# Performance work log

Measured on AMD Instinct MI355X. Metric: run time of the kernel, lower is better.

The kernel has to match this reference:

```python
import jax, jax.numpy as jnp
import numpy as np

B, N, D, F_IN, E, RATIO, C, HEADS, KERNELS = 128, 512, 128, 128, 524288, 128, 10, 4, 3
ALPHA = 0.5


def setup_inputs() -> dict:
    key = jax.random.key(0)
    ks = jax.random.split(key, 20)

    def w(k, shape, fan):
        return (jax.random.normal(k, shape, jnp.float32) / np.float32(np.sqrt(fan)))

    gid = jnp.arange(E, dtype=jnp.int32) // (E // B)
    src = gid * N + jax.random.randint(ks[0], (E,), 0, N, dtype=jnp.int32)
    dst = gid * N + jax.random.randint(ks[1], (E,), 0, N, dtype=jnp.int32)
    edge_index = jnp.stack([src, dst]).astype(jnp.int32)
    return {
        'x': jax.random.normal(ks[2], (B * N, F_IN), jnp.float32),
        'edge_index': edge_index,
        'enc_w': w(ks[3], (F_IN, D), F_IN), 'enc_b': jnp.zeros((D,), jnp.float32),
        'gconv_w': w(ks[4], (3, KERNELS, D, D), D), 'gconv_b': jnp.zeros((3, KERNELS, D), jnp.float32),
        'wg1_w': w(ks[5], (D,), D), 'wg1_b': jnp.zeros((1,), jnp.float32),
        'wg2_w': w(ks[6], (D,), D), 'wg2_b': jnp.zeros((1,), jnp.float32),
        'pg1_w': w(ks[7], (D,), D), 'pg1_b': jnp.zeros((1,), jnp.float32),
        'pg2_w': w(ks[8], (D,), D), 'pg2_b': jnp.zeros((1,), jnp.float32),
        'q_w': w(ks[9], (D, D), D), 'q_b': jnp.zeros((D,), jnp.float32),
        'k_w': w(ks[10], (D, D), D), 'k_b': jnp.zeros((D,), jnp.float32),
        'v_w': w(ks[11], (D, D), D), 'v_b': jnp.zeros((D,), jnp.float32),
        'o_w': w(ks[12], (D, D), D), 'o_b': jnp.zeros((D,), jnp.float32),
        'ro_w': w(ks[13], (RATIO,), RATIO), 'ro_b': jnp.zeros((1,), jnp.float32),
        'c1_w': w(ks[14], (D, D), D), 'c1_b': jnp.zeros((D,), jnp.float32),
        'c2_w': w(ks[15], (D, C), D), 'c2_b': jnp.zeros((C,), jnp.float32),
    }


def _make_gcn(edge_index, n):
    # PyG GCNConv: add self-loops, symmetric normalization D^-1/2 (A+I) D^-1/2
    src, dst = edge_index[0], edge_index[1]
    deg = jax.ops.segment_sum(jnp.ones(src.shape[0], jnp.float32), dst, num_segments=n) + 1.0
    dinv = jax.lax.rsqrt(deg)
    norm = dinv[src] * dinv[dst]          # [E]
    self_norm = dinv * dinv               # self-loop coefficient

    def gcn(x, W, b):
        h = x @ W                                                  # [n, out]
        out = jax.ops.segment_sum(h[src] * norm[:, None], dst, num_segments=n)
        return out + h * self_norm[:, None] + b
    return gcn


def _forward(x, edge_index, enc_w, enc_b, gconv_w, gconv_b,
             wg1_w, wg1_b, wg2_w, wg2_b, pg1_w, pg1_b, pg2_w, pg2_b,
             q_w, q_b, k_w, k_b, v_w, v_b, o_w, o_b, ro_w, ro_b,
             c1_w, c1_b, c2_w, c2_b):
    n = x.shape[0]
    gcn = _make_gcn(edge_index, n)
    h = x @ enc_w + enc_b                   # node encoder (dropout: eval mode)

    def mkgc(hin, Ws, bs):                  # sum of relu(GCNConv) over kernels
        out = jax.nn.relu(gcn(hin, Ws[0], bs[0]))
        for kk in range(1, Ws.shape[0]):
            out = out + jax.nn.relu(gcn(hin, Ws[kk], bs[kk]))
        return out

    x1 = mkgc(h, gconv_w[0], gconv_b[0])
    x2 = mkgc(x1, gconv_w[1], gconv_b[1])
    x3 = mkgc(x2, gconv_w[2], gconv_b[2])

    def gla_score(xi, w1, b1, w2, b2):      # GLAPool(flag=1): global + local score
        s1 = xi @ w1[:, None] + b1          # [n,1]
        s2 = gcn(xi, w2[:, None], b2)       # [n,1]
        return ALPHA * s1 + (1.0 - ALPHA) * s2

    wts = jnp.concatenate([gla_score(xi, wg1_w, wg1_b, wg2_w, wg2_b)
                           for xi in (x1, x2, x3)], axis=-1)        # [n,3]
    wts = jax.nn.softmax(wts, axis=-1)
    xf = wts[:, 0:1] * x1 + wts[:, 1:2] * x2 + wts[:, 2:3] * x3

    # GLAPool top-k pooling (uniform graph sizes -> dense [B,N])
    score = gla_score(xf, pg1_w, pg1_b, pg2_w, pg2_b)[:, 0].reshape(B, N)
    vals, idx = jax.lax.top_k(score, RATIO)                          # [B,RATIO]
    xd = xf.reshape(B, N, D)
    xp = jnp.take_along_axis(xd, idx[:, :, None], axis=1) * jnp.tanh(vals)[:, :, None]

    # MAB: Q from pooled nodes, K/V = GCNConv over full graph
    dh = D // HEADS
    Qh = (xp @ q_w + q_b).reshape(B, RATIO, HEADS, dh)
    K = gcn(xf, k_w, k_b).reshape(B, N, HEADS, dh)
    V = gcn(xf, v_w, v_b).reshape(B, N, HEADS, dh)
    att = jnp.einsum('bqhd,bkhd->bhqk', Qh, K) / jnp.sqrt(jnp.float32(D))
    A = jax.nn.softmax(att, axis=-1)
    O = Qh + jnp.einsum('bhqk,bkhd->bqhd', A, V)
    O = O.reshape(B, RATIO, D)
    O = O + jax.nn.relu(O @ o_w + o_b)

    # Conv1d(ratio, 1, 1) readout == learned weighted sum over pooled slots
    xg = jnp.einsum('r,brd->bd', ro_w, O) + ro_b                     # [B,D]

    hc = jax.nn.relu(xg @ c1_w + c1_b)
    logp = jax.nn.log_softmax(hc @ c2_w + c2_b, axis=-1)
    return logp, xg


def reference(x, edge_index, enc_w, enc_b, gconv_w, gconv_b,
              wg1_w, wg1_b, wg2_w, wg2_b, pg1_w, pg1_b, pg2_w, pg2_b,
              q_w, q_b, k_w, k_b, v_w, v_b, o_w, o_b, ro_w, ro_b,
              c1_w, c1_b, c2_w, c2_b):
    return _forward(x, edge_index, enc_w, enc_b, gconv_w, gconv_b,
                    wg1_w, wg1_b, wg2_w, wg2_b, pg1_w, pg1_b, pg2_w, pg2_b,
                    q_w, q_b, k_w, k_b, v_w, v_b, o_w, o_b, ro_w, ro_b,
                    c1_w, c1_b, c2_w, c2_b)
```

## Files before the change

kernel.cpp:

```cpp
#include <hip/hip_runtime.h>
#include <math.h>

#define N_NODES 65536
#define NE      524288
#define DD      128
#define BGRAPH  128
#define NPG     512
#define RATIO_K 128
#define NHEAD   4
#define DHEAD   32

typedef short bf16x8 __attribute__((ext_vector_type(8)));
typedef float f32x4 __attribute__((ext_vector_type(4)));

union U8 { unsigned short u[8]; bf16x8 v; };
union U4x { unsigned q[4]; bf16x8 v; };

__device__ __forceinline__ unsigned short f2b(float f) {
  unsigned u = __float_as_uint(f);
  unsigned r = u + 0x7fffu + ((u >> 16) & 1u);
  return (unsigned short)(r >> 16);
}
__device__ __forceinline__ float b2f(unsigned short h) {
  return __uint_as_float(((unsigned)h) << 16);
}
__device__ __forceinline__ void split3t(float v, unsigned short& h, unsigned short& m, unsigned short& l) {
  unsigned u = __float_as_uint(v);
  h = (unsigned short)(u >> 16);
  float vm = v - __uint_as_float(u & 0xffff0000u);
  unsigned um = __float_as_uint(vm);
  m = (unsigned short)(um >> 16);
  float vl = vm - __uint_as_float(um & 0xffff0000u);
  l = (unsigned short)(__float_as_uint(vl) >> 16);
}


__global__ void count_kernel(const int* __restrict__ dst, int* __restrict__ cnt) {
  int e = blockIdx.x * 256 + threadIdx.x;
  if (e < NE) atomicAdd(&cnt[dst[e]], 1);
}

__global__ void dinv_kernel(const int* __restrict__ cnt, float* __restrict__ dinv) {
  int i = blockIdx.x * 256 + threadIdx.x;
  if (i < N_NODES) dinv[i] = rsqrtf((float)cnt[i] + 1.0f);
}

__global__ __launch_bounds__(512) void scan_kernel2(const int* __restrict__ cnt, int* __restrict__ rp) {
  __shared__ int part[512];
  int g = blockIdx.x, t = threadIdx.x;
  int v = cnt[g * 512 + t];
  part[t] = v;
  __syncthreads();
  for (int off = 1; off < 512; off <<= 1) {
    int u = (t >= off) ? part[t - off] : 0;
    __syncthreads();
    part[t] += u;
    __syncthreads();
  }
  rp[g * 512 + t] = g * 4096 + part[t] - v;
  if (g == BGRAPH - 1 && t == 511) rp[N_NODES] = NE;
}

__global__ void scatter_kernel(const int* __restrict__ edge, const int* __restrict__ rp,
                               int* __restrict__ fill, const float* __restrict__ dinv,
                               int* __restrict__ col, float* __restrict__ wgt) {
  int e = blockIdx.x * 256 + threadIdx.x;
  if (e >= NE) return;
  int s = edge[e];
  int d = edge[NE + e];
  int p = rp[d] + atomicAdd(&fill[d], 1);
  col[p] = s;
  wgt[p] = dinv[s] * dinv[d];
}

struct WPtrs { const float* p[14]; };

__global__ void wprep_all(WPtrs wp, unsigned short* __restrict__ dstBase) {
  int mat = blockIdx.y;
  int idx = blockIdx.x * 256 + threadIdx.x;
  const float* __restrict__ W = wp.p[mat];
  unsigned short* __restrict__ dst = dstBase + (size_t)mat * 49152;
  int k = idx >> 7, n = idx & 127;
  float v = W[k * 128 + n];
  unsigned short h, m, l;
  split3t(v, h, m, l);
  dst[n * 128 + k] = h;
  dst[16384 + n * 128 + k] = m;
  dst[32768 + n * 128 + k] = l;
}

#define WROW 36

template<int NW, bool RELU, bool RES, bool DUAL, bool DOT>
__global__ __launch_bounds__(256, 2) void mfma_gemm8(
    const float* __restrict__ A,
    const unsigned short* __restrict__ Wt,
    const float* __restrict__ bias, const float* __restrict__ bias2,
    const float* __restrict__ res,
    float* __restrict__ out, float* __restrict__ out2,
    const float* __restrict__ dw1, const float* __restrict__ dw2,
    float* __restrict__ t1g, float* __restrict__ t2g) {
  __shared__ unsigned short Wlds[NW * 3 * 64 * WROW];
  int tid = threadIdx.x;
  int wave = tid >> 6, lane = tid & 63;
  int c16 = lane & 15, kg = lane >> 4;
  int wrow = (wave >> 1) * 32;
  int wcol = (wave & 1) * 32;
  size_t row0 = (size_t)blockIdx.y * 64 + wrow;
  int n0 = blockIdx.x * 64;

  f32x4 acc[NW][2][2];
  #pragma unroll
  for (int m = 0; m < NW; ++m)
    #pragma unroll
    for (int mi = 0; mi < 2; ++mi)
      #pragma unroll
      for (int ni = 0; ni < 2; ++ni) acc[m][mi][ni] = (f32x4){0.f, 0.f, 0.f, 0.f};

  for (int ks = 0; ks < 4; ++ks) {
    if (ks) __syncthreads();
    #pragma unroll
    for (int i = 0; i < NW * 3; ++i) {
      int c = tid + i * 256;
      int u4 = c & 3;
      int n = (c >> 2) & 63;
      int mp = c >> 8;
      *(uint4*)&Wlds[(mp * 64 + n) * WROW + u4 * 8] =
          *(const uint4*)&Wt[(size_t)mp * 16384 + (n0 + n) * 128 + ks * 32 + u4 * 8];
    }
    __syncthreads();

    bf16x8 a[2][3];
    #pragma unroll
    for (int mi = 0; mi < 2; ++mi) {
      const float* ap = A + (row0 + mi * 16 + c16) * 128 + ks * 32 + kg * 8;
      float4 f0 = *(const float4*)ap;
      float4 f1 = *(const float4*)(ap + 4);
      float f[8] = {f0.x, f0.y, f0.z, f0.w, f1.x, f1.y, f1.z, f1.w};
      U4x hh, mm, ll;
      #pragma unroll
      for (int p = 0; p < 4; ++p) {
        float v0 = f[2 * p], v1 = f[2 * p + 1];
        unsigned u0 = __float_as_uint(v0), u1 = __float_as_uint(v1);
        unsigned u1m = u1 & 0xffff0000u;
        hh.q[p] = (u0 >> 16) | u1m;
        float m0 = v0 - __uint_as_float(u0 & 0xffff0000u);
        float m1 = v1 - __uint_as_float(u1m);
        unsigned w0 = __float_as_uint(m0), w1 = __float_as_uint(m1);
        unsigned w1m = w1 & 0xffff0000u;
        mm.q[p] = (w0 >> 16) | w1m;
        float l0 = m0 - __uint_as_float(w0 & 0xffff0000u);
        float l1 = m1 - __uint_as_float(w1m);
        ll.q[p] = (__float_as_uint(l0) >> 16) | (__float_as_uint(l1) & 0xffff0000u);
      }
      a[mi][0] = hh.v; a[mi][1] = mm.v; a[mi][2] = ll.v;
    }

    #pragma unroll
    for (int mat = 0; mat < NW; ++mat) {
      #pragma unroll
      for (int ni = 0; ni < 2; ++ni) {
        int nrow = (wcol >> 4) + ni;
        int off = ((mat * 3) * 64 + nrow * 16 + c16) * WROW + kg * 8;
        bf16x8 bh = *(const bf16x8*)&Wlds[off];
        bf16x8 bm = *(const bf16x8*)&Wlds[off + 64 * WROW];
        bf16x8 bl = *(const bf16x8*)&Wlds[off + 128 * WROW];
        #pragma unroll
        for (int mi = 0; mi < 2; ++mi) {
          acc[mat][mi][ni] = __builtin_amdgcn_mfma_f32_16x16x32_bf16(a[mi][0], bh, acc[mat][mi][ni], 0, 0, 0);
          acc[mat][mi][ni] = __builtin_amdgcn_mfma_f32_16x16x32_bf16(a[mi][0], bm, acc[mat][mi][ni], 0, 0, 0);
          acc[mat][mi][ni] = __builtin_amdgcn_mfma_f32_16x16x32_bf16(a[mi][1], bh, acc[mat][mi][ni], 0, 0, 0);
          acc[mat][mi][ni] = __builtin_amdgcn_mfma_f32_16x16x32_bf16(a[mi][0], bl, acc[mat][mi][ni], 0, 0, 0);
          acc[mat][mi][ni] = __builtin_amdgcn_mfma_f32_16x16x32_bf16(a[mi][2], bh, acc[mat][mi][ni], 0, 0, 0);
          acc[mat][mi][ni] = __builtin_amdgcn_mfma_f32_16x16x32_bf16(a[mi][1], bm, acc[mat][mi][ni], 0, 0, 0);
        }
      }
    }
  }

  float s1a[2][4], s2a[2][4];
  if (DOT) {
    #pragma unroll
    for (int mi = 0; mi < 2; ++mi)
      #pragma unroll
      for (int r = 0; r < 4; ++r) { s1a[mi][r] = 0.f; s2a[mi][r] = 0.f; }
  }
  #pragma unroll
  for (int mi = 0; mi < 2; ++mi)
    #pragma unroll
    for (int ni = 0; ni < 2; ++ni) {
      int colg = n0 + wcol + ni * 16 + c16;
      float w1c = 0.f, w2c = 0.f;
      if (DOT) { w1c = dw1[colg]; w2c = dw2[colg]; }
      #pragma unroll
      for (int r = 0; r < 4; ++r) {
        size_t o = (row0 + mi * 16 + kg * 4 + r) * 128 + colg;
        if (DUAL) {
          out[o]  = acc[0][mi][ni][r] + bias[colg];
          out2[o] = acc[NW - 1][mi][ni][r] + bias2[colg];
        } else if (NW == 3) {
          float g = fmaxf(acc[0][mi][ni][r] + bias[colg], 0.f)
                  + fmaxf(acc[1][mi][ni][r] + bias[128 + colg], 0.f)
                  + fmaxf(acc[2][mi][ni][r] + bias[256 + colg], 0.f);
          out[o] = g;
          if (DOT) { s1a[mi][r] += g * w1c; s2a[mi][r] += g * w2c; }
        } else {
          float g = acc[0][mi][ni][r] + bias[colg];
          if (RELU) g = fmaxf(g, 0.f);
          if (RES) g += res[o];
          out[o] = g;
        }
      }
    }
  if (DOT) {
    #pragma unroll
    for (int mi = 0; mi < 2; ++mi)
      #pragma unroll
      for (int r = 0; r < 4; ++r) {
        float v1 = s1a[mi][r], v2 = s2a[mi][r];
        v1 += __shfl_xor(v1, 1);  v2 += __shfl_xor(v2, 1);
        v1 += __shfl_xor(v1, 2);  v2 += __shfl_xor(v2, 2);
        v1 += __shfl_xor(v1, 4);  v2 += __shfl_xor(v2, 4);
        v1 += __shfl_xor(v1, 8);  v2 += __shfl_xor(v2, 8);
        if (c16 == 0) {
          size_t row = row0 + mi * 16 + kg * 4 + r;
          atomicAdd(&t1g[row], v1);
          atomicAdd(&t2g[row], v2);
        }
      }
  }
}

__global__ __launch_bounds__(256) void gemm_k128(
    const float* __restrict__ A, const float* __restrict__ W,
    const float* __restrict__ bias, const float* __restrict__ res,
    float* __restrict__ out, int M, int do_relu) {
  __shared__ float As[8][64];
  __shared__ float Ws[8][128];
  int tid = threadIdx.x;
  int tx = tid & 15;
  int ty = tid >> 4;
  int row0 = blockIdx.x * 64;
  if (row0 >= M) return;
  const float* Ab = A + (size_t)row0 * DD;

  float acc[4][8];
  #pragma unroll
  for (int i = 0; i < 4; ++i)
    #pragma unroll
    for (int j = 0; j < 8; ++j) acc[i][j] = 0.f;

  for (int k0 = 0; k0 < 128; k0 += 8) {
    {
      int e = tid * 2;
      int r = e >> 3, kk = e & 7;
      float2 av = *(const float2*)&Ab[r * DD + k0 + kk];
      As[kk][r] = av.x;
      As[kk + 1][r] = av.y;
    }
    {
      int kk = tid >> 5, c = (tid & 31) * 4;
      float4 wv = *(const float4*)&W[(k0 + kk) * DD + c];
      *(float4*)&Ws[kk][c] = wv;
    }
    __syncthreads();
    #pragma unroll
    for (int kk = 0; kk < 8; ++kk) {
      float4 a4 = *(const float4*)&As[kk][ty * 4];
      float4 b0 = *(const float4*)&Ws[kk][tx * 8];
      float4 b1 = *(const float4*)&Ws[kk][tx * 8 + 4];
      float av[4] = {a4.x, a4.y, a4.z, a4.w};
      float bv[8] = {b0.x, b0.y, b0.z, b0.w, b1.x, b1.y, b1.z, b1.w};
      #pragma unroll
      for (int i = 0; i < 4; ++i)
        #pragma unroll
        for (int j = 0; j < 8; ++j) acc[i][j] += av[i] * bv[j];
    }
    __syncthreads();
  }
  #pragma unroll
  for (int i = 0; i < 4; ++i) {
    int r = row0 + ty * 4 + i;
    size_t base = (size_t)r * DD + tx * 8;
    #pragma unroll
    for (int j = 0; j < 8; ++j) {
      float g = acc[i][j];
      if (bias) g += bias[tx * 8 + j];
      if (do_relu) g = fmaxf(g, 0.f);
      if (res) g += res[base + j];
      out[base + j] = g;
    }
  }
}

__global__ __launch_bounds__(256) void agg4_kernel(
    const float* __restrict__ H, const int* __restrict__ rp, const int* __restrict__ col,
    const float* __restrict__ wgt, const float* __restrict__ dinv,
    float* __restrict__ out) {
  int g = blockIdx.x * 256 + threadIdx.x;
  int node = g >> 5;
  int l = g & 31;
  const float4* H4 = (const float4*)H;
  float dv = dinv[node];
  float4 acc = H4[(size_t)node * 32 + l];
  float sn = dv * dv;
  acc.x *= sn; acc.y *= sn; acc.z *= sn; acc.w *= sn;
  int beg = rp[node], end = rp[node + 1];
  for (int j = beg; j < end; ++j) {
    float w = wgt[j];
    int c = col[j];
    float4 hv = H4[(size_t)c * 32 + l];
    acc.x += w * hv.x; acc.y += w * hv.y; acc.z += w * hv.z; acc.w += w * hv.w;
  }
  ((float4*)out)[(size_t)node * 32 + l] = acc;
}

__global__ void score_kernel(const float* __restrict__ t1, const float* __restrict__ t2,
                             const int* __restrict__ rp, const int* __restrict__ col,
                             const float* __restrict__ wgt, const float* __restrict__ dinv,
                             const float* __restrict__ b1p, const float* __restrict__ b2p,
                             float* __restrict__ out) {
  int i = blockIdx.x * 256 + threadIdx.x;
  if (i >= N_NODES) return;
  float dv = dinv[i];
  float a2 = dv * dv * t2[i] + b2p[0];
  int beg = rp[i], end = rp[i + 1];
  for (int j = beg; j < end; ++j) a2 += wgt[j] * t2[col[j]];
  out[i] = 0.5f * (t1[i] + b1p[0]) + 0.5f * a2;
}

__global__ void xf_kernel(const float* __restrict__ x1, const float* __restrict__ x2,
                          const float* __restrict__ x3, const float* __restrict__ sc,
                          const float* __restrict__ w1, const float* __restrict__ w2,
                          float* __restrict__ xf, float* __restrict__ t1, float* __restrict__ t2) {
  size_t idx = (size_t)blockIdx.x * 256 + threadIdx.x;
  int i = (int)(idx >> 5);
  float s0 = sc[i], s1 = sc[N_NODES + i], s2 = sc[2 * N_NODES + i];
  float mx = fmaxf(s0, fmaxf(s1, s2));
  float e0 = __expf(s0 - mx), e1 = __expf(s1 - mx), e2 = __expf(s2 - mx);
  float inv = 1.f / (e0 + e1 + e2);
  e0 *= inv; e1 *= inv; e2 *= inv;
  float4 a = ((const float4*)x1)[idx];
  float4 b = ((const float4*)x2)[idx];
  float4 c = ((const float4*)x3)[idx];
  float4 o;
  o.x = e0 * a.x + e1 * b.x + e2 * c.x;
  o.y = e0 * a.y + e1 * b.y + e2 * c.y;
  o.z = e0 * a.z + e1 * b.z + e2 * c.z;
  o.w = e0 * a.w + e1 * b.w + e2 * c.w;
  ((float4*)xf)[idx] = o;

  int l = (int)(idx & 31);
  float4 w1v = ((const float4*)w1)[l];
  float4 w2v = ((const float4*)w2)[l];
  float d1 = o.x * w1v.x + o.y * w1v.y + o.z * w1v.z + o.w * w1v.w;
  float d2 = o.x * w2v.x + o.y * w2v.y + o.z * w2v.z + o.w * w2v.w;
  #pragma unroll
  for (int off = 1; off <= 16; off <<= 1) {
    d1 += __shfl_xor(d1, off);
    d2 += __shfl_xor(d2, off);
  }
  if (l == 0) { t1[i] = d1; t2[i] = d2; }
}

__global__ __launch_bounds__(512) void topk_kernel(const float* __restrict__ score,
                                                   int* __restrict__ idxO, float* __restrict__ valO) {
  int b = blockIdx.x;
  int t = threadIdx.x;
  __shared__ float s[512];
  float v = score[b * NPG + t];
  s[t] = v;
  __syncthreads();
  int rank = 0;
  for (int j = 0; j < 512; ++j) {
    float u = s[j];
    rank += (u > v) || (u == v && j < t);
  }
  if (rank < RATIO_K) { idxO[b * RATIO_K + rank] = t; valO[b * RATIO_K + rank] = v; }
}

__global__ void xp_kernel(const float* __restrict__ xf, const int* __restrict__ idx,
                          const float* __restrict__ vals, float* __restrict__ xp) {
  size_t e = (size_t)blockIdx.x * 256 + threadIdx.x;
  int b = (int)(e >> 14);
  int r = (int)((e >> 7) & 127);
  int f = (int)(e & 127);
  float tv = tanhf(vals[b * RATIO_K + r]);
  int node = idx[b * RATIO_K + r];
  xp[e] = xf[((size_t)b * NPG + node) * DD + f] * tv;
}

__global__ __launch_bounds__(256) void attn_mfma_kernel(
    const float* __restrict__ Q, const float* __restrict__ K,
    const float* __restrict__ V, float* __restrict__ O) {
  int bb = blockIdx.x >> 2, h = blockIdx.x & 3;
  int tid = threadIdx.x;
  int wave = tid >> 6, lane = tid & 63;
  int c16 = lane & 15, kg = lane >> 4;
  int qbase = wave * 32;
  const float cscale = 0.088388347648318447f;

  __shared__ float Vs[64][34];
  __shared__ unsigned char PwB[4][32 * 144];

  bf16x8 Qh[2], Ql[2];
  #pragma unroll
  for (int qt = 0; qt < 2; ++qt) {
    const float* qp = Q + ((size_t)bb * 128 + qbase + qt * 16 + c16) * 128 + h * 32 + kg * 8;
    float4 f0 = *(const float4*)qp;
    float4 f1 = *(const float4*)(qp + 4);
    float f[8] = {f0.x, f0.y, f0.z, f0.w, f1.x, f1.y, f1.z, f1.w};
    U8 hh, ll;
    #pragma unroll
    for (int j = 0; j < 8; ++j) { hh.u[j] = f2b(f[j]); ll.u[j] = f2b(f[j] - b2f(hh.u[j])); }
    Qh[qt] = hh.v; Ql[qt] = ll.v;
  }

  float m2[2] = {-3.0e38f, -3.0e38f};
  float l2[2] = {0.f, 0.f};
  f32x4 od[2][2];
  #pragma unroll
  for (int dt = 0; dt < 2; ++dt)
    #pragma unroll
    for (int qt = 0; qt < 2; ++qt) od[dt][qt] = (f32x4){0.f, 0.f, 0.f, 0.f};

  for (int kc = 0; kc < NPG; kc += 64) {
    if (kc) __syncthreads();
    {
      int j = tid >> 2, grp = tid & 3;
      const float* vp = V + ((size_t)bb * NPG + kc + j) * 128 + h * 32 + grp * 8;
      float4 v0 = *(const float4*)vp;
      float4 v1 = *(const float4*)(vp + 4);
      float* d = &Vs[j][grp * 8];
      *(float2*)&d[0] = make_float2(v0.x, v0.y);
      *(float2*)&d[2] = make_float2(v0.z, v0.w);
      *(float2*)&d[4] = make_float2(v1.x, v1.y);
      *(float2*)&d[6] = make_float2(v1.z, v1.w);
    }
    __syncthreads();

    f32x4 sac[2][4];
    #pragma unroll
    for (int qt = 0; qt < 2; ++qt)
      #pragma unroll
      for (int kt = 0; kt < 4; ++kt) sac[qt][kt] = (f32x4){0.f, 0.f, 0.f, 0.f};

    #pragma unroll
    for (int kt = 0; kt < 4; ++kt) {
      const float* kp = K + ((size_t)bb * NPG + kc + kt * 16 + c16) * 128 + h * 32 + kg * 8;
      float4 f0 = *(const float4*)kp;
      float4 f1 = *(const float4*)(kp + 4);
      float f[8] = {f0.x, f0.y, f0.z, f0.w, f1.x, f1.y, f1.z, f1.w};
      U8 hh, ll;
      #pragma unroll
      for (int j = 0; j < 8; ++j) { hh.u[j] = f2b(f[j]); ll.u[j] = f2b(f[j] - b2f(hh.u[j])); }
      #pragma unroll
      for (int qt = 0; qt < 2; ++qt) {
        sac[qt][kt] = __builtin_amdgcn_mfma_f32_16x16x32_bf16(hh.v, Qh[qt], sac[qt][kt], 0, 0, 0);
        sac[qt][kt] = __builtin_amdgcn_mfma_f32_16x16x32_bf16(hh.v, Ql[qt], sac[qt][kt], 0, 0, 0);
        sac[qt][kt] = __builtin_amdgcn_mfma_f32_16x16x32_bf16(ll.v, Qh[qt], sac[qt][kt], 0, 0, 0);
      }
    }

    float pj[2][16];
    float scl2[2];
    #pragma unroll
    for (int qt = 0; qt < 2; ++qt) {
      float mc = -3.0e38f;
      #pragma unroll
      for (int kt = 0; kt < 4; ++kt)
        #pragma unroll
        for (int r = 0; r < 4; ++r) {
          float v = sac[qt][kt][r] * cscale;
          pj[qt][kt * 4 + r] = v;
          mc = fmaxf(mc, v);
        }
      mc = fmaxf(mc, __shfl_xor(mc, 16));
      mc = fmaxf(mc, __shfl_xor(mc, 32));
      float mnew = fmaxf(m2[qt], mc);
      float scl = __expf(m2[qt] - mnew);
      float ls = 0.f;
      #pragma unroll
      for (int i = 0; i < 16; ++i) {
        float e = __expf(pj[qt][i] - mnew);
        pj[qt][i] = e;
        ls += e;
      }
      ls += __shfl_xor(ls, 16);
      ls += __shfl_xor(ls, 32);
      l2[qt] = l2[qt] * scl + ls;
      m2[qt] = mnew;
      scl2[qt] = scl;
    }
    #pragma unroll
    for (int dt = 0; dt < 2; ++dt)
      #pragma unroll
      for (int qt = 0; qt < 2; ++qt) {
        #pragma unroll
        for (int r = 0; r < 4; ++r) od[dt][qt][r] *= scl2[qt];
      }

    #pragma unroll
    for (int qt = 0; qt < 2; ++qt) {
      int q32 = qt * 16 + c16;
      unsigned char* pb = &PwB[wave][q32 * 144];
      unsigned sw = (unsigned)((q32 & 7) << 4);
      #pragma unroll
      for (int kt = 0; kt < 4; ++kt)
        #pragma unroll
        for (int rp = 0; rp < 2; ++rp) {
          unsigned pk = (unsigned)f2b(pj[qt][kt * 4 + 2 * rp]) |
                        ((unsigned)f2b(pj[qt][kt * 4 + 2 * rp + 1]) << 16);
          *(unsigned*)&pb[((unsigned)(kt * 32 + kg * 8 + 4 * rp)) ^ sw] = pk;
        }
    }

    #pragma unroll
    for (int kw = 0; kw < 2; ++kw) {
      bf16x8 Pb[2];
      #pragma unroll
      for (int qt = 0; qt < 2; ++qt) {
        int q32 = qt * 16 + c16;
        Pb[qt] = *(const bf16x8*)&PwB[wave][q32 * 144 +
                   (((unsigned)(kw * 64 + kg * 16)) ^ ((unsigned)((q32 & 7) << 4)))];
      }
      #pragma unroll
      for (int dt = 0; dt < 2; ++dt) {
        U8 vh, vl;
        #pragma unroll
        for (int j = 0; j < 8; ++j) {
          float v = Vs[kw * 32 + kg * 8 + j][dt * 16 + c16];
          vh.u[j] = f2b(v);
          vl.u[j] = f2b(v - b2f(vh.u[j]));
        }
        #pragma unroll
        for (int qt = 0; qt < 2; ++qt) {
          od[dt][qt] = __builtin_amdgcn_mfma_f32_16x16x32_bf16(vh.v, Pb[qt], od[dt][qt], 0, 0, 0);
          od[dt][qt] = __builtin_amdgcn_mfma_f32_16x16x32_bf16(vl.v, Pb[qt], od[dt][qt], 0, 0, 0);
        }
      }
    }
  }

  #pragma unroll
  for (int qt = 0; qt < 2; ++qt) {
    float inv = 1.f / l2[qt];
    size_t row = (size_t)bb * 128 + qbase + qt * 16 + c16;
    #pragma unroll
    for (int dt = 0; dt < 2; ++dt)
      #pragma unroll
      for (int r = 0; r < 4; ++r) {
        int colg = h * 32 + dt * 16 + kg * 4 + r;
        O[row * 128 + colg] = Q[row * 128 + colg] + od[dt][qt][r] * inv;
      }
  }
}

__global__ void readout_kernel(const float* __restrict__ O2, const float* __restrict__ ro_w,
                               const float* __restrict__ ro_b, float* __restrict__ xg) {
  int idx = blockIdx.x * 256 + threadIdx.x;
  int b = idx >> 7, d = idx & 127;
  float s = ro_b[0];
  for (int r = 0; r < RATIO_K; ++r) s += ro_w[r] * O2[((size_t)b * RATIO_K + r) * DD + d];
  xg[idx] = s;
}

__global__ __launch_bounds__(64) void head_kernel(const float* __restrict__ hc,
                                                  const float* __restrict__ c2w,
                                                  const float* __restrict__ c2b,
                                                  float* __restrict__ out) {
  int b = blockIdx.x, t = threadIdx.x;
  __shared__ float z[10];
  __shared__ float lse_s;
  if (t < 10) {
    float s = c2b[t];
    for (int k = 0; k < 128; ++k) s += hc[b * 128 + k] * c2w[k * 10 + t];
    z[t] = s;
  }
  __syncthreads();
  if (t == 0) {
    float mx = z[0];
    for (int c = 1; c < 10; ++c) mx = fmaxf(mx, z[c]);
    float sum = 0.f;
    for (int c = 0; c < 10; ++c) sum += expf(z[c] - mx);
    lse_s = mx + logf(sum);
  }
  __syncthreads();
  if (t < 10) out[b * 10 + t] = z[t] - lse_s;
}

extern "C" void kernel_launch(void* const* d_in, const int* in_sizes, int n_in,
                              void* d_out, int out_size, void* d_ws, size_t ws_size,
                              hipStream_t stream) {
  const float* x       = (const float*)d_in[0];
  const int*   edge    = (const int*)d_in[1];
  const float* enc_w   = (const float*)d_in[2];
  const float* enc_b   = (const float*)d_in[3];
  const float* gconv_w = (const float*)d_in[4];
  const float* gconv_b = (const float*)d_in[5];
  const float* wg1_w   = (const float*)d_in[6];
  const float* wg1_b   = (const float*)d_in[7];
  const float* wg2_w   = (const float*)d_in[8];
  const float* wg2_b   = (const float*)d_in[9];
  const float* pg1_w   = (const float*)d_in[10];
  const float* pg1_b   = (const float*)d_in[11];
  const float* pg2_w   = (const float*)d_in[12];
  const float* pg2_b   = (const float*)d_in[13];
  const float* q_w     = (const float*)d_in[14];
  const float* q_b     = (const float*)d_in[15];
  const float* k_w     = (const float*)d_in[16];
  const float* k_b     = (const float*)d_in[17];
  const float* v_w     = (const float*)d_in[18];
  const float* v_b     = (const float*)d_in[19];
  const float* o_w     = (const float*)d_in[20];
  const float* o_b     = (const float*)d_in[21];
  const float* ro_w    = (const float*)d_in[22];
  const float* ro_b    = (const float*)d_in[23];
  const float* c1_w    = (const float*)d_in[24];
  const float* c1_b    = (const float*)d_in[25];
  const float* c2_w    = (const float*)d_in[26];
  const float* c2_b    = (const float*)d_in[27];

  float* outp = (float*)d_out;

  const size_t S = (size_t)N_NODES * DD;
  float* ws    = (float*)d_ws;
  float* slot0 = ws;
  float* slot1 = ws + S;
  float* slot2 = ws + 2 * S;
  float* slot3 = ws + 3 * S;
  float* smallf = ws + 4 * S;
  int*   cnt  = (int*)smallf;
  int*   fill = cnt + N_NODES;
  int*   rp   = fill + N_NODES;
  int*   col  = rp + N_NODES + 8;
  float* wgt  = (float*)(col + NE);
  float* dinv = wgt + NE;
  float* sc   = dinv + N_NODES;
  float* t1   = sc + 3 * N_NODES;
  float* t2   = t1 + N_NODES;
  float* score = t2 + N_NODES;
  int*   tidx = (int*)(score + N_NODES);
  float* tval = (float*)(tidx + BGRAPH * RATIO_K);
  float* hcbuf = tval + BGRAPH * RATIO_K;
  unsigned short* wsW = (unsigned short*)(hcbuf + BGRAPH * DD);
  float* aggbuf = (float*)(wsW + 14 * 49152);

  const size_t SP = (size_t)BGRAPH * RATIO_K * DD;
  float* xp = slot3;
  float* Qm = slot3 + SP;
  float* Om = slot3 + 2 * SP;
  float* O2 = slot3 + 3 * SP;

  hipMemsetAsync(cnt, 0, N_NODES * sizeof(int), stream);
  hipMemsetAsync(fill, 0, N_NODES * sizeof(int), stream);
  count_kernel<<<NE / 256, 256, 0, stream>>>(edge + NE, cnt);
  dinv_kernel<<<N_NODES / 256, 256, 0, stream>>>(cnt, dinv);
  scan_kernel2<<<BGRAPH, 512, 0, stream>>>(cnt, rp);
  scatter_kernel<<<NE / 256, 256, 0, stream>>>(edge, rp, fill, dinv, col, wgt);

  WPtrs wp;
  wp.p[0] = enc_w;
  for (int i = 0; i < 9; ++i) wp.p[1 + i] = gconv_w + (size_t)i * DD * DD;
  wp.p[10] = k_w; wp.p[11] = v_w; wp.p[12] = q_w; wp.p[13] = o_w;
  wprep_all<<<dim3(64, 14), 256, 0, stream>>>(wp, wsW);

  mfma_gemm8<1, false, false, false, false><<<dim3(2, 1024), 256, 0, stream>>>(
      x, wsW, enc_b, nullptr, nullptr, slot0, nullptr, nullptr, nullptr, nullptr, nullptr);

  float* lin[4] = {slot0, slot1, slot2, slot3};
  const int AGG_GRID = (N_NODES * 32) / 256;
  for (int l = 0; l < 3; ++l) {
    const float* hin = lin[l];
    float* hout = lin[l + 1];
    agg4_kernel<<<AGG_GRID, 256, 0, stream>>>(hin, rp, col, wgt, dinv, aggbuf);
    hipMemsetAsync(t1, 0, N_NODES * sizeof(float), stream);
    hipMemsetAsync(t2, 0, N_NODES * sizeof(float), stream);
    mfma_gemm8<3, true, false, false, true><<<dim3(2, 1024), 256, 0, stream>>>(
        aggbuf, wsW + (size_t)(1 + l * 3) * 49152, gconv_b + (size_t)l * 3 * DD,
        nullptr, nullptr, hout, nullptr, wg1_w, wg2_w, t1, t2);
    score_kernel<<<N_NODES / 256, 256, 0, stream>>>(t1, t2, rp, col, wgt, dinv, wg1_b, wg2_b, sc + (size_t)l * N_NODES);
  }

  float* xf = slot0;
  xf_kernel<<<(N_NODES * 32) / 256, 256, 0, stream>>>(slot1, slot2, slot3, sc, pg1_w, pg2_w, xf, t1, t2);

  score_kernel<<<N_NODES / 256, 256, 0, stream>>>(t1, t2, rp, col, wgt, dinv, pg1_b, pg2_b, score);
  topk_kernel<<<BGRAPH, 512, 0, stream>>>(score, tidx, tval);
  xp_kernel<<<(BGRAPH * RATIO_K * DD) / 256, 256, 0, stream>>>(xf, tidx, tval, xp);

  mfma_gemm8<1, false, false, false, false><<<dim3(2, 256), 256, 0, stream>>>(
      xp, wsW + 12 * 49152UL, q_b, nullptr, nullptr, Qm, nullptr, nullptr, nullptr, nullptr, nullptr);

  agg4_kernel<<<AGG_GRID, 256, 0, stream>>>(xf, rp, col, wgt, dinv, aggbuf);
  mfma_gemm8<2, false, false, true, false><<<dim3(2, 1024), 256, 0, stream>>>(
      aggbuf, wsW + 10 * 49152UL, k_b, v_b, nullptr, slot1, slot2, nullptr, nullptr, nullptr, nullptr);

  attn_mfma_kernel<<<BGRAPH * NHEAD, 256, 0, stream>>>(Qm, slot1, slot2, Om);

  mfma_gemm8<1, true, true, false, false><<<dim3(2, 256), 256, 0, stream>>>(
      Om, wsW + 13 * 49152UL, o_b, nullptr, Om, O2, nullptr, nullptr, nullptr, nullptr, nullptr);

  float* xg = outp + BGRAPH * 10;
  readout_kernel<<<(BGRAPH * DD) / 256, 256, 0, stream>>>(O2, ro_w, ro_b, xg);

  gemm_k128<<<BGRAPH / 64, 256, 0, stream>>>(xg, c1_w, c1_b, nullptr, hcbuf, BGRAPH, 1);
  head_kernel<<<BGRAPH, 64, 0, stream>>>(hcbuf, c2_w, c2_b, outp);
}
```

Baseline: 652.7 us.

## Fuse score, gather, readout and classifier stages into neighboring kernels

Fuses the per-layer score computation into the next layer's aggregation kernel, and folds the top-k gather-and-scale into the Q GEMM's A-load. It also folds the readout weighted sum into the O GEMM epilogue via atomics, and merges the classifier GEMM and head into one kernel. The pooled-feature aggregation is reused for the K/V GEMM, which removes a duplicate agg pass. Intermediate buffers and several launches and memsets are eliminated, at the cost of atomic accumulation order changes and extra per-edge score loads.

Measured after the change: 616.1 us. 5.6% less time.

```diff
diff --git a/kernel.cpp b/kernel.cpp
--- a/kernel.cpp
+++ b/kernel.cpp
@@ -91,7 +91,7 @@
 
 #define WROW 36
 
-template<int NW, bool RELU, bool RES, bool DUAL, bool DOT>
+template<int NW, bool RELU, bool RES, bool DUAL, bool DOT, bool GATHER, bool RDOUT>
 __global__ __launch_bounds__(256, 2) void mfma_gemm8(
     const float* __restrict__ A,
     const unsigned short* __restrict__ Wt,
@@ -99,7 +99,9 @@
     const float* __restrict__ res,
     float* __restrict__ out, float* __restrict__ out2,
     const float* __restrict__ dw1, const float* __restrict__ dw2,
-    float* __restrict__ t1g, float* __restrict__ t2g) {
+    float* __restrict__ t1g, float* __restrict__ t2g,
+    const int* __restrict__ tidxp, const float* __restrict__ tvalp,
+    const float* __restrict__ ro_w, float* __restrict__ xg) {
   __shared__ unsigned short Wlds[NW * 3 * 64 * WROW];
   int tid = threadIdx.x;
   int wave = tid >> 6, lane = tid & 63;
@@ -109,6 +111,22 @@
   size_t row0 = (size_t)blockIdx.y * 64 + wrow;
   int n0 = blockIdx.x * 64;
 
+  const float* arow[2];
+  float ascale[2];
+  #pragma unroll
+  for (int mi = 0; mi < 2; ++mi) {
+    size_t gr = row0 + mi * 16 + c16;
+    if (GATHER) {
+      int b = (int)(gr >> 7);
+      int node = tidxp[gr];
+      arow[mi] = A + ((size_t)b * NPG + node) * DD;
+      ascale[mi] = tanhf(tvalp[gr]);
+    } else {
+      arow[mi] = A + gr * DD;
+      ascale[mi] = 1.f;
+    }
+  }
+
   f32x4 acc[NW][2][2];
   #pragma unroll
   for (int m = 0; m < NW; ++m)
@@ -133,10 +151,14 @@
     bf16x8 a[2][3];
     #pragma unroll
     for (int mi = 0; mi < 2; ++mi) {
-      const float* ap = A + (row0 + mi * 16 + c16) * 128 + ks * 32 + kg * 8;
+      const float* ap = arow[mi] + ks * 32 + kg * 8;
       float4 f0 = *(const float4*)ap;
       float4 f1 = *(const float4*)(ap + 4);
       float f[8] = {f0.x, f0.y, f0.z, f0.w, f1.x, f1.y, f1.z, f1.w};
+      if (GATHER) {
+        #pragma unroll
+        for (int j = 0; j < 8; ++j) f[j] *= ascale[mi];
+      }
       U4x hh, mm, ll;
       #pragma unroll
       for (int p = 0; p < 4; ++p) {
@@ -185,6 +207,7 @@
       #pragma unroll
       for (int r = 0; r < 4; ++r) { s1a[mi][r] = 0.f; s2a[mi][r] = 0.f; }
   }
+  float rdo[2][2];
   #pragma unroll
   for (int mi = 0; mi < 2; ++mi)
     #pragma unroll
@@ -192,6 +215,7 @@
       int colg = n0 + wcol + ni * 16 + c16;
       float w1c = 0.f, w2c = 0.f;
       if (DOT) { w1c = dw1[colg]; w2c = dw2[colg]; }
+      if (RDOUT) rdo[mi][ni] = 0.f;
       #pragma unroll
       for (int r = 0; r < 4; ++r) {
         size_t o = (row0 + mi * 16 + kg * 4 + r) * 128 + colg;
@@ -208,8 +232,17 @@
           float g = acc[0][mi][ni][r] + bias[colg];
           if (RELU) g = fmaxf(g, 0.f);
           if (RES) g += res[o];
-          out[o] = g;
+          if (RDOUT) {
+            int slot = (int)((row0 + mi * 16 + kg * 4 + r) & 127);
+            rdo[mi][ni] += ro_w[slot] * g;
+          } else {
+            out[o] = g;
+          }
         }
+      }
+      if (RDOUT) {
+        int b = (int)(row0 >> 7);
+        atomicAdd(&xg[b * 128 + colg], rdo[mi][ni]);
       }
     }
   if (DOT) {
@@ -231,72 +264,14 @@
   }
 }
 
-__global__ __launch_bounds__(256) void gemm_k128(
-    const float* __restrict__ A, const float* __restrict__ W,
-    const float* __restrict__ bias, const float* __restrict__ res,
-    float* __restrict__ out, int M, int do_relu) {
-  __shared__ float As[8][64];
-  __shared__ float Ws[8][128];
-  int tid = threadIdx.x;
-  int tx = tid & 15;
-  int ty = tid >> 4;
-  int row0 = blockIdx.x * 64;
-  if (row0 >= M) return;
-  const float* Ab = A + (size_t)row0 * DD;
-
-  float acc[4][8];
-  #pragma unroll
-  for (int i = 0; i < 4; ++i)
-    #pragma unroll
-    for (int j = 0; j < 8; ++j) acc[i][j] = 0.f;
-
-  for (int k0 = 0; k0 < 128; k0 += 8) {
-    {
-      int e = tid * 2;
-      int r = e >> 3, kk = e & 7;
-      float2 av = *(const float2*)&Ab[r * DD + k0 + kk];
-      As[kk][r] = av.x;
-      As[kk + 1][r] = av.y;
-    }
-    {
-      int kk = tid >> 5, c = (tid & 31) * 4;
-      float4 wv = *(const float4*)&W[(k0 + kk) * DD + c];
-      *(float4*)&Ws[kk][c] = wv;
-    }
-    __syncthreads();
-    #pragma unroll
-    for (int kk = 0; kk < 8; ++kk) {
-      float4 a4 = *(const float4*)&As[kk][ty * 4];
-      float4 b0 = *(const float4*)&Ws[kk][tx * 8];
-      float4 b1 = *(const float4*)&Ws[kk][tx * 8 + 4];
-      float av[4] = {a4.x, a4.y, a4.z, a4.w};
-      float bv[8] = {b0.x, b0.y, b0.z, b0.w, b1.x, b1.y, b1.z, b1.w};
-      #pragma unroll
-      for (int i = 0; i < 4; ++i)
-        #pragma unroll
-        for (int j = 0; j < 8; ++j) acc[i][j] += av[i] * bv[j];
-    }
-    __syncthreads();
-  }
-  #pragma unroll
-  for (int i = 0; i < 4; ++i) {
-    int r = row0 + ty * 4 + i;
-    size_t base = (size_t)r * DD + tx * 8;
-    #pragma unroll
-    for (int j = 0; j < 8; ++j) {
-      float g = acc[i][j];
-      if (bias) g += bias[tx * 8 + j];
-      if (do_relu) g = fmaxf(g, 0.f);
-      if (res) g += res[base + j];
-      out[base + j] = g;
-    }
-  }
-}
-
+template<bool SCORE>
 __global__ __launch_bounds__(256) void agg4_kernel(
     const float* __restrict__ H, const int* __restrict__ rp, const int* __restrict__ col,
     const float* __restrict__ wgt, const float* __restrict__ dinv,
-    float* __restrict__ out) {
+    float* __restrict__ out,
+    const float* __restrict__ t1s, const float* __restrict__ t2s,
+    const float* __restrict__ b1p, const float* __restrict__ b2p,
+    float* __restrict__ scoreOut) {
   int g = blockIdx.x * 256 + threadIdx.x;
   int node = g >> 5;
   int l = g & 31;
@@ -305,14 +280,20 @@
   float4 acc = H4[(size_t)node * 32 + l];
   float sn = dv * dv;
   acc.x *= sn; acc.y *= sn; acc.z *= sn; acc.w *= sn;
+  float s2 = 0.f;
   int beg = rp[node], end = rp[node + 1];
   for (int j = beg; j < end; ++j) {
     float w = wgt[j];
     int c = col[j];
     float4 hv = H4[(size_t)c * 32 + l];
     acc.x += w * hv.x; acc.y += w * hv.y; acc.z += w * hv.z; acc.w += w * hv.w;
+    if (SCORE) { if (l == 0) s2 += w * t2s[c]; }
   }
   ((float4*)out)[(size_t)node * 32 + l] = acc;
+  if (SCORE && l == 0) {
+    float a2 = sn * t2s[node] + b2p[0] + s2;
+    scoreOut[node] = 0.5f * (t1s[node] + b1p[0]) + 0.5f * a2;
+  }
 }
 
 __global__ void score_kernel(const float* __restrict__ t1, const float* __restrict__ t2,
@@ -379,17 +360,6 @@
   if (rank < RATIO_K) { idxO[b * RATIO_K + rank] = t; valO[b * RATIO_K + rank] = v; }
 }
 
-__global__ void xp_kernel(const float* __restrict__ xf, const int* __restrict__ idx,
-                          const float* __restrict__ vals, float* __restrict__ xp) {
-  size_t e = (size_t)blockIdx.x * 256 + threadIdx.x;
-  int b = (int)(e >> 14);
-  int r = (int)((e >> 7) & 127);
-  int f = (int)(e & 127);
-  float tv = tanhf(vals[b * RATIO_K + r]);
-  int node = idx[b * RATIO_K + r];
-  xp[e] = xf[((size_t)b * NPG + node) * DD + f] * tv;
-}
-
 __global__ __launch_bounds__(256) void attn_mfma_kernel(
     const float* __restrict__ Q, const float* __restrict__ K,
     const float* __restrict__ V, float* __restrict__ O) {
@@ -556,26 +526,29 @@
   }
 }
 
-__global__ void readout_kernel(const float* __restrict__ O2, const float* __restrict__ ro_w,
-                               const float* __restrict__ ro_b, float* __restrict__ xg) {
-  int idx = blockIdx.x * 256 + threadIdx.x;
-  int b = idx >> 7, d = idx & 127;
-  float s = ro_b[0];
-  for (int r = 0; r < RATIO_K; ++r) s += ro_w[r] * O2[((size_t)b * RATIO_K + r) * DD + d];
-  xg[idx] = s;
-}
-
-__global__ __launch_bounds__(64) void head_kernel(const float* __restrict__ hc,
-                                                  const float* __restrict__ c2w,
-                                                  const float* __restrict__ c2b,
-                                                  float* __restrict__ out) {
+__global__ void xg_init_kernel(float* __restrict__ xg, const float* __restrict__ ro_b) {
+  int i = blockIdx.x * 256 + threadIdx.x;
+  if (i < BGRAPH * DD) xg[i] = ro_b[0];
+}
+
+__global__ __launch_bounds__(128) void clshead_kernel(
+    const float* __restrict__ xg, const float* __restrict__ c1w, const float* __restrict__ c1b,
+    const float* __restrict__ c2w, const float* __restrict__ c2b, float* __restrict__ out) {
   int b = blockIdx.x, t = threadIdx.x;
+  __shared__ float xr[128];
+  __shared__ float hc[128];
   __shared__ float z[10];
   __shared__ float lse_s;
+  xr[t] = xg[b * 128 + t];
+  __syncthreads();
+  float s = c1b[t];
+  for (int k = 0; k < 128; ++k) s += xr[k] * c1w[k * 128 + t];
+  hc[t] = fmaxf(s, 0.f);
+  __syncthreads();
   if (t < 10) {
-    float s = c2b[t];
-    for (int k = 0; k < 128; ++k) s += hc[b * 128 + k] * c2w[k * 10 + t];
-    z[t] = s;
+    float s2 = c2b[t];
+    for (int k = 0; k < 128; ++k) s2 += hc[k] * c2w[k * 10 + t];
+    z[t] = s2;
   }
   __syncthreads();
   if (t == 0) {
@@ -637,23 +610,30 @@
   float* wgt  = (float*)(col + NE);
   float* dinv = wgt + NE;
   float* sc   = dinv + N_NODES;
-  float* t1   = sc + 3 * N_NODES;
-  float* t2   = t1 + N_NODES;
-  float* score = t2 + N_NODES;
+  float* tb   = sc + 3 * N_NODES;
+  float* score = tb + 8 * N_NODES;
   int*   tidx = (int*)(score + N_NODES);
   float* tval = (float*)(tidx + BGRAPH * RATIO_K);
-  float* hcbuf = tval + BGRAPH * RATIO_K;
-  unsigned short* wsW = (unsigned short*)(hcbuf + BGRAPH * DD);
+  float* xg   = tval + BGRAPH * RATIO_K;
+  unsigned short* wsW = (unsigned short*)(xg + BGRAPH * DD);
   float* aggbuf = (float*)(wsW + 14 * 49152);
 
+  float* t1_0 = tb;
+  float* t2_0 = tb + N_NODES;
+  float* t1_1 = tb + 2 * N_NODES;
+  float* t2_1 = tb + 3 * N_NODES;
+  float* t1_2 = tb + 4 * N_NODES;
+  float* t2_2 = tb + 5 * N_NODES;
+  float* t1_p = tb + 6 * N_NODES;
+  float* t2_p = tb + 7 * N_NODES;
+
   const size_t SP = (size_t)BGRAPH * RATIO_K * DD;
-  float* xp = slot3;
   float* Qm = slot3 + SP;
   float* Om = slot3 + 2 * SP;
-  float* O2 = slot3 + 3 * SP;
 
   hipMemsetAsync(cnt, 0, N_NODES * sizeof(int), stream);
   hipMemsetAsync(fill, 0, N_NODES * sizeof(int), stream);
+  hipMemsetAsync(tb, 0, 8 * N_NODES * sizeof(float), stream);
   count_kernel<<<NE / 256, 256, 0, stream>>>(edge + NE, cnt);
   dinv_kernel<<<N_NODES / 256, 256, 0, stream>>>(cnt, dinv);
   scan_kernel2<<<BGRAPH, 512, 0, stream>>>(cnt, rp);
@@ -665,45 +645,58 @@
   wp.p[10] = k_w; wp.p[11] = v_w; wp.p[12] = q_w; wp.p[13] = o_w;
   wprep_all<<<dim3(64, 14), 256, 0, stream>>>(wp, wsW);
 
-  mfma_gemm8<1, false, false, false, false><<<dim3(2, 1024), 256, 0, stream>>>(
-      x, wsW, enc_b, nullptr, nullptr, slot0, nullptr, nullptr, nullptr, nullptr, nullptr);
-
+  mfma_gemm8<1, false, false, false, false, false, false><<<dim3(2, 1024), 256, 0, stream>>>(
+      x, wsW, enc_b, nullptr, nullptr, slot0, nullptr,
+      nullptr, nullptr, nullptr, nullptr, nullptr, nullptr, nullptr, nullptr);
+
+  const int AGG_GRID = (N_NODES * 32) / 256;
   float* lin[4] = {slot0, slot1, slot2, slot3};
-  const int AGG_GRID = (N_NODES * 32) / 256;
-  for (int l = 0; l < 3; ++l) {
-    const float* hin = lin[l];
-    float* hout = lin[l + 1];
-    agg4_kernel<<<AGG_GRID, 256, 0, stream>>>(hin, rp, col, wgt, dinv, aggbuf);
-    hipMemsetAsync(t1, 0, N_NODES * sizeof(float), stream);
-    hipMemsetAsync(t2, 0, N_NODES * sizeof(float), stream);
-    mfma_gemm8<3, true, false, false, true><<<dim3(2, 1024), 256, 0, stream>>>(
+  float* t1s[3] = {t1_0, t1_1, t1_2};
+  float* t2s[3] = {t2_0, t2_1, t2_2};
+
+  agg4_kernel<false><<<AGG_GRID, 256, 0, stream>>>(
+      lin[0], rp, col, wgt, dinv, aggbuf, nullptr, nullptr, nullptr, nullptr, nullptr);
+  mfma_gemm8<3, true, false, false, true, false, false><<<dim3(2, 1024), 256, 0, stream>>>(
+      aggbuf, wsW + 1 * 49152UL, gconv_b, nullptr, nullptr, lin[1], nullptr,
+      wg1_w, wg2_w, t1_0, t2_0, nullptr, nullptr, nullptr, nullptr);
+
+  for (int l = 1; l < 3; ++l) {
+    agg4_kernel<true><<<AGG_GRID, 256, 0, stream>>>(
+        lin[l], rp, col, wgt, dinv, aggbuf,
+        t1s[l - 1], t2s[l - 1], wg1_b, wg2_b, sc + (size_t)(l - 1) * N_NODES);
+    mfma_gemm8<3, true, false, false, true, false, false><<<dim3(2, 1024), 256, 0, stream>>>(
         aggbuf, wsW + (size_t)(1 + l * 3) * 49152, gconv_b + (size_t)l * 3 * DD,
-        nullptr, nullptr, hout, nullptr, wg1_w, wg2_w, t1, t2);
-    score_kernel<<<N_NODES / 256, 256, 0, stream>>>(t1, t2, rp, col, wgt, dinv, wg1_b, wg2_b, sc + (size_t)l * N_NODES);
-  }
+        nullptr, nullptr, lin[l + 1], nullptr,
+        wg1_w, wg2_w, t1s[l], t2s[l], nullptr, nullptr, nullptr, nullptr);
+  }
+
+  score_kernel<<<N_NODES / 256, 256, 0, stream>>>(t1_2, t2_2, rp, col, wgt, dinv, wg1_b, wg2_b, sc + 2 * (size_t)N_NODES);
 
   float* xf = slot0;
-  xf_kernel<<<(N_NODES * 32) / 256, 256, 0, stream>>>(slot1, slot2, slot3, sc, pg1_w, pg2_w, xf, t1, t2);
-
-  score_kernel<<<N_NODES / 256, 256, 0, stream>>>(t1, t2, rp, col, wgt, dinv, pg1_b, pg2_b, score);
+  xf_kernel<<<(N_NODES * 32) / 256, 256, 0, stream>>>(slot1, slot2, slot3, sc, pg1_w, pg2_w, xf, t1_p, t2_p);
+
+  agg4_kernel<true><<<AGG_GRID, 256, 0, stream>>>(
+      xf, rp, col, wgt, dinv, aggbuf, t1_p, t2_p, pg1_b, pg2_b, score);
+
   topk_kernel<<<BGRAPH, 512, 0, stream>>>(score, tidx, tval);
-  xp_kernel<<<(BGRAPH * RATIO_K * DD) / 256, 256, 0, stream>>>(xf, tidx, tval, xp);
-
-  mfma_gemm8<1, false, false, false, false><<<dim3(2, 256), 256, 0, stream>>>(
-      xp, wsW + 12 * 49152UL, q_b, nullptr, nullptr, Qm, nullptr, nullptr, nullptr, nullptr, nullptr);
-
-  agg4_kernel<<<AGG_GRID, 256, 0, stream>>>(xf, rp, col, wgt, dinv, aggbuf);
-  mfma_gemm8<2, false, false, true, false><<<dim3(2, 1024), 256, 0, stream>>>(
-      aggbuf, wsW + 10 * 49152UL, k_b, v_b, nullptr, slot1, slot2, nullptr, nullptr, nullptr, nullptr);
+
+  mfma_gemm8<1, false, false, false, false, true, false><<<dim3(2, 256), 256, 0, stream>>>(
+      xf, wsW + 12 * 49152UL, q_b, nullptr, nullptr, Qm, nullptr,
+      nullptr, nullptr, nullptr, nullptr, tidx, tval, nullptr, nullptr);
+
+  mfma_gemm8<2, false, false, true, false, false, false><<<dim3(2, 1024), 256, 0, stream>>>(
+      aggbuf, wsW + 10 * 49152UL, k_b, v_b, nullptr, slot1, slot2,
+      nullptr, nullptr, nullptr, nullptr, nullptr, nullptr, nullptr, nullptr);
 
   attn_mfma_kernel<<<BGRAPH * NHEAD, 256, 0, stream>>>(Qm, slot1, slot2, Om);
 
-  mfma_gemm8<1, true, true, false, false><<<dim3(2, 256), 256, 0, stream>>>(
-      Om, wsW + 13 * 49152UL, o_b, nullptr, Om, O2, nullptr, nullptr, nullptr, nullptr, nullptr);
-
-  float* xg = outp + BGRAPH * 10;
-  readout_kernel<<<(BGRAPH * DD) / 256, 256, 0, stream>>>(O2, ro_w, ro_b, xg);
-
-  gemm_k128<<<BGRAPH / 64, 256, 0, stream>>>(xg, c1_w, c1_b, nullptr, hcbuf, BGRAPH, 1);
-  head_kernel<<<BGRAPH, 64, 0, stream>>>(hcbuf, c2_w, c2_b, outp);
-}
+  xg_init_kernel<<<(BGRAPH * DD) / 256, 256, 0, stream>>>(xg, ro_b);
+  mfma_gemm8<1, true, true, false, false, false, true><<<dim3(2, 256), 256, 0, stream>>>(
+      Om, wsW + 13 * 49152UL, o_b, nullptr, Om, nullptr, nullptr,
+      nullptr, nullptr, nullptr, nullptr, nullptr, nullptr, ro_w, xg);
+
+  hipMemcpyAsync(outp + BGRAPH * 10, xg, BGRAPH * DD * sizeof(float),
+                 hipMemcpyDeviceToDevice, stream);
+
+  clshead_kernel<<<BGRAPH, 128, 0, stream>>>(xg, c1_w, c1_b, c2_w, c2_b, outp);
+}
```
